# Kernel optimization log

Measured on AMD Instinct MI355X. Metric: run time of the kernel, lower is better.

## Reference

```python
import jax, jax.numpy as jnp
import numpy as np
import math

B, T, D = 2, 1024, 1024
H, K = 16, 64
THETA = 0.5
LAYER_ID, N_LAYERS = 4, 12
D_MIX, D_DECAY = 32, 64
LN_EPS = 1e-5 * 8.0 ** 2  # eps = 1e-5 * head_size_divisor**2


def setup_inputs() -> dict:
    key = jax.random.key(0)
    ks = jax.random.split(key, 10)
    x = jax.random.normal(ks[0], (B, T, D), jnp.float32)

    r01 = LAYER_ID / max(N_LAYERS - 1, 1)
    r1a0 = 1.0 - LAYER_ID / N_LAYERS
    ddd = (jnp.arange(D, dtype=jnp.float32) / D).reshape(1, 1, D)
    time_maa_x = 1.0 - ddd ** r1a0
    time_maa_w = 1.0 - ddd ** r1a0
    time_maa_k = 1.0 - ddd ** r1a0
    time_maa_v = 1.0 - (ddd ** r1a0 + 0.3 * r01)
    time_maa_r = 1.0 - ddd ** (0.5 * r1a0)
    time_maa_g = 1.0 - ddd ** (0.5 * r1a0)
    time_maa_w1 = jax.random.normal(ks[1], (D, D_MIX * 5), jnp.float32) * 0.01
    time_maa_w2 = jax.random.uniform(ks[2], (5, D_MIX, D), jnp.float32, -0.01, 0.01)

    n = jnp.arange(D, dtype=jnp.float32)
    time_decay = (-6.0 + 5.0 * (n / (D - 1)) ** (0.7 + 1.3 * r01)).reshape(1, 1, D)
    time_decay_w1 = jax.random.normal(ks[3], (D, D_DECAY), jnp.float32) * 0.01
    time_decay_w2 = jax.random.uniform(ks[4], (D_DECAY, D), jnp.float32, -0.01, 0.01)

    s = 1.0 / math.sqrt(D)
    W_r = jax.random.normal(ks[5], (D, D), jnp.float32) * s
    W_k = jax.random.normal(ks[6], (D, D), jnp.float32) * s
    W_v = jax.random.normal(ks[7], (D, D), jnp.float32) * s
    W_g = jax.random.normal(ks[8], (D, D), jnp.float32) * s
    W_o = jax.random.normal(ks[9], (D, D), jnp.float32) * s
    ln_gamma = jnp.ones((D,), jnp.float32)
    ln_beta = jnp.zeros((D,), jnp.float32)

    return dict(x=x, time_maa_x=time_maa_x, time_maa_w=time_maa_w,
                time_maa_k=time_maa_k, time_maa_v=time_maa_v,
                time_maa_r=time_maa_r, time_maa_g=time_maa_g,
                time_maa_w1=time_maa_w1, time_maa_w2=time_maa_w2,
                time_decay=time_decay, time_decay_w1=time_decay_w1,
                time_decay_w2=time_decay_w2, W_r=W_r, W_k=W_k, W_v=W_v,
                W_g=W_g, W_o=W_o, ln_gamma=ln_gamma, ln_beta=ln_beta)


def _bidir_token_shift(x):
    # bidirectional token shift: mean of previous and next token (zero-padded)
    prev = jnp.concatenate([jnp.zeros_like(x[:, :1]), x[:, :-1]], axis=1)
    nxt = jnp.concatenate([x[:, 1:], jnp.zeros_like(x[:, :1])], axis=1)
    return 0.5 * (prev + nxt)


def _lion_complex_attention(r, k, v, w, theta):
    # r,k,v,w: (B,H,T,K). Effective mask M[i,j] = exp-decay^|i-j| * cos(theta*|i-j|)
    cs = jnp.cumsum(w, axis=2)
    cs_b = cs - w
    cf = jnp.clip(cs - cs[:, :, T // 2:T // 2 + 1, :], -60.0, 60.0)
    cb = jnp.clip(cs_b - cs_b[:, :, T // 2:T // 2 + 1, :], -60.0, 60.0)
    t_idx = jnp.arange(T, dtype=jnp.float32)
    thF = (theta * (t_idx + 1.0)).reshape(1, 1, T, 1)
    thB = (theta * t_idx).reshape(1, 1, T, 1)
    exp_f, exp_nf = jnp.exp(cf), jnp.exp(-cf)
    exp_b, exp_nb = jnp.exp(cb), jnp.exp(-cb)
    mm = lambda a, b: jnp.einsum('bhik,bhjk->bhij', a, b)
    A_fwd = jnp.tril(mm(r * exp_f * jnp.cos(thF), k * exp_nf * jnp.cos(thF))
                     + mm(r * exp_f * jnp.sin(thF), k * exp_nf * jnp.sin(thF)))
    A_bwd = jnp.triu(mm(r * exp_nb * jnp.cos(thB), k * exp_b * jnp.cos(thB))
                     + mm(r * exp_nb * jnp.sin(thB), k * exp_b * jnp.sin(thB)), k=1)
    return (A_fwd + A_bwd) @ v  # (B,H,T,K)


def reference(x, time_maa_x, time_maa_w, time_maa_k, time_maa_v, time_maa_r,
              time_maa_g, time_maa_w1, time_maa_w2, time_decay, time_decay_w1,
              time_decay_w2, W_r, W_k, W_v, W_g, W_o, ln_gamma, ln_beta):
    dxprev = _bidir_token_shift(x) - x
    xxx = x + dxprev * time_maa_x
    t5 = jnp.tanh(xxx @ time_maa_w1).reshape(B, T, 5, D_MIX)
    m = jnp.einsum('btfm,fmd->fbtd', t5, time_maa_w2)  # (5,B,T,D)
    mw, mk, mv, mr, mg = m[0], m[1], m[2], m[3], m[4]
    xw = x + dxprev * (time_maa_w + mw)
    xk = x + dxprev * (time_maa_k + mk)
    xv = x + dxprev * (time_maa_v + mv)
    xr = x + dxprev * (time_maa_r + mr)
    xg = x + dxprev * (time_maa_g + mg)

    r = xr @ W_r
    k = xk @ W_k
    v = xv @ W_v
    g = jax.nn.silu(xg @ W_g)
    w = time_decay + jnp.tanh(xw @ time_decay_w1) @ time_decay_w2

    heads = lambda a: a.reshape(B, T, H, K).transpose(0, 2, 1, 3)
    r_h, k_h, v_h = heads(r), heads(k), heads(v)
    w_h = jnp.minimum(-jnp.exp(heads(w)), math.log(0.99))

    y = _lion_complex_attention(r_h, k_h, v_h, w_h, THETA)  # (B,H,T,K)
    y = y.transpose(0, 2, 1, 3).reshape(B * T, D)

    # GroupNorm(n_head groups) over channels
    yg = y.reshape(B * T, H, K)
    mu = yg.mean(axis=-1, keepdims=True)
    var = yg.var(axis=-1, keepdims=True)
    yn = ((yg - mu) / jnp.sqrt(var + LN_EPS)).reshape(B * T, D)
    y = (yn * ln_gamma + ln_beta).reshape(B, T, D)

    return (y * g) @ W_o
```

## Files before the change

### kernel.cpp

```cpp
#include <hip/hip_runtime.h>
#include <hip/hip_bf16.h>

using u16 = unsigned short;
using bf16x8 = __attribute__((ext_vector_type(8))) __bf16;
using f32x4  = __attribute__((ext_vector_type(4))) float;
using u16x4  = __attribute__((ext_vector_type(4))) u16;

#define DEV static __device__ __forceinline__

constexpr int Tn = 1024, Dn = 1024;

DEV u16 f2b(float f) { union { __hip_bfloat16 h; u16 u; } cv; cv.h = __float2bfloat16(f); return cv.u; }
DEV float b2f(u16 u) { union { unsigned i; float f; } cv; cv.i = (unsigned)u << 16; return cv.f; }
DEV void lds16(const void* g, void* s) {
    __builtin_amdgcn_global_load_lds(
        (const __attribute__((address_space(1))) void*)g,
        (__attribute__((address_space(3))) void*)s, 16, 0, 0);
}

__global__ __launch_bounds__(256) void k_shift(const float* __restrict__ x, const float* __restrict__ maa_x,
                                               float* __restrict__ dxp, u16* __restrict__ xxx) {
    long i4 = ((long)blockIdx.x * 256 + threadIdx.x) * 4;
    int t = (int)((i4 >> 10) & (Tn - 1));
    f32x4 xc = *(const f32x4*)(x + i4);
    f32x4 xp = {0.f, 0.f, 0.f, 0.f}, xn = {0.f, 0.f, 0.f, 0.f};
    if (t > 0)      xp = *(const f32x4*)(x + i4 - Dn);
    if (t < Tn - 1) xn = *(const f32x4*)(x + i4 + Dn);
    f32x4 dx = 0.5f * (xp + xn) - xc;
    *(f32x4*)(dxp + i4) = dx;
    f32x4 mx = *(const f32x4*)(maa_x + (i4 & (Dn - 1)));
    f32x4 v = xc + dx * mx;
    u16x4 o;
#pragma unroll
    for (int j = 0; j < 4; j++) o[j] = f2b(v[j]);
    *(u16x4*)(xxx + i4) = o;
}

__global__ __launch_bounds__(256) void k_transpose(const float* __restrict__ in,
                                                   u16* __restrict__ out, int R, int C) {
    __shared__ float tile[32][33];
    int c0 = blockIdx.x * 32, r0 = blockIdx.y * 32;
    int tx = threadIdx.x & 31, ty = threadIdx.x >> 5;
#pragma unroll
    for (int i = 0; i < 4; i++)
        tile[ty + i * 8][tx] = in[(long)(r0 + ty + i * 8) * C + c0 + tx];
    __syncthreads();
#pragma unroll
    for (int i = 0; i < 4; i++)
        out[(long)(c0 + ty + i * 8) * R + r0 + tx] = f2b(tile[tx][ty + i * 8]);
}

struct P5 { const float* p[5]; };
__global__ __launch_bounds__(256) void k_transpose5(P5 in, u16* __restrict__ out) {
    const float* src = in.p[blockIdx.z];
    u16* dst = out + (long)blockIdx.z * 1024 * 1024;
    __shared__ float tile[32][33];
    int c0 = blockIdx.x * 32, r0 = blockIdx.y * 32;
    int tx = threadIdx.x & 31, ty = threadIdx.x >> 5;
#pragma unroll
    for (int i = 0; i < 4; i++)
        tile[ty + i * 8][tx] = src[(long)(r0 + ty + i * 8) * 1024 + c0 + tx];
    __syncthreads();
#pragma unroll
    for (int i = 0; i < 4; i++)
        dst[(long)(c0 + ty + i * 8) * 1024 + r0 + tx] = f2b(tile[tx][ty + i * 8]);
}

enum { EPI_F32 = 0, EPI_TANH_F32, EPI_RKVG_BF16, EPI_TANH_BF16, EPI_DECAY_F32 };

template <int EPI, bool LOA = false>
__global__ __launch_bounds__(256) void k_gemm(const u16* __restrict__ A, const u16* __restrict__ A2,
                                              const u16* __restrict__ Bt,
                                              void* __restrict__ Cv, int M, int N, int K,
                                              long bA, long bB, long bC,
                                              const float* __restrict__ bias) {
    const u16* Ab = A + (long)blockIdx.z * bA;
    const u16* Bb = Bt + (long)blockIdx.z * bB;
    __shared__ __align__(16) u16 As[128 * 64];
    __shared__ __align__(16) u16 As2[LOA ? 128 * 64 : 8];
    __shared__ __align__(16) u16 Bs[128 * 64];
    int m0 = blockIdx.x * 128, n0 = blockIdx.y * 128;
    int tid = threadIdx.x, lane = tid & 63, wv = tid >> 6;
    int wm = (wv >> 1) * 64, wn = (wv & 1) * 64;
    f32x4 acc[4][4] = {};
    for (int k0 = 0; k0 < K; k0 += 64) {
        __syncthreads();
#pragma unroll
        for (int i = 0; i < 4; i++) {
            int c = tid + i * 256;
            int row = c >> 3;
            int grp = (c & 7) ^ (row & 7);
            long off = (long)row * K + k0 + grp * 8;
            lds16(Ab + (long)m0 * K + off, As + c * 8);
            if constexpr (LOA) lds16(A2 + (long)m0 * K + off, As2 + c * 8);
            lds16(Bb + (long)n0 * K + off, Bs + c * 8);
        }
        __syncthreads();
#pragma unroll
        for (int ksub = 0; ksub < 2; ksub++) {
            bf16x8 af[4], af2[4], bfv[4];
#pragma unroll
            for (int q = 0; q < 4; q++) {
                int row = wm + q * 16 + (lane & 15);
                int idx = (row * 64 + ksub * 32 + (lane >> 4) * 8) ^ ((row & 7) << 3);
                af[q] = *(const bf16x8*)(As + idx);
                if constexpr (LOA) af2[q] = *(const bf16x8*)(As2 + idx);
            }
#pragma unroll
            for (int q = 0; q < 4; q++) {
                int row = wn + q * 16 + (lane & 15);
                int idx = (row * 64 + ksub * 32 + (lane >> 4) * 8) ^ ((row & 7) << 3);
                bfv[q] = *(const bf16x8*)(Bs + idx);
            }
#pragma unroll
            for (int i = 0; i < 4; i++)
#pragma unroll
                for (int j = 0; j < 4; j++) {
                    acc[i][j] = __builtin_amdgcn_mfma_f32_16x16x32_bf16(af[i], bfv[j], acc[i][j], 0, 0, 0);
                    if constexpr (LOA)
                        acc[i][j] = __builtin_amdgcn_mfma_f32_16x16x32_bf16(af2[i], bfv[j], acc[i][j], 0, 0, 0);
                }
        }
    }
#pragma unroll
    for (int i = 0; i < 4; i++)
#pragma unroll
        for (int j = 0; j < 4; j++)
#pragma unroll
            for (int r = 0; r < 4; r++) {
                int gr = m0 + wm + i * 16 + ((lane >> 4) << 2) + r;
                int gc = n0 + wn + j * 16 + (lane & 15);
                if (gc < N) {
                    float v = acc[i][j][r];
                    long off = (long)blockIdx.z * bC + (long)gr * N + gc;
                    if constexpr (EPI == EPI_F32) ((float*)Cv)[off] = v;
                    else if constexpr (EPI == EPI_TANH_F32) ((float*)Cv)[off] = tanhf(v);
                    else if constexpr (EPI == EPI_RKVG_BF16) {
                        ((u16*)Cv)[off] = f2b((blockIdx.z == 3) ? v / (1.f + expf(-v)) : v);
                    }
                    else if constexpr (EPI == EPI_TANH_BF16) ((u16*)Cv)[off] = f2b(tanhf(v));
                    else if constexpr (EPI == EPI_DECAY_F32) {
                        float w = v + bias[gc];
                        ((float*)Cv)[off] = fminf(-expf(w), -0.010050335853501451f);
                    }
                }
            }
}

__global__ __launch_bounds__(256) void k_mixer(const float* __restrict__ x, const float* __restrict__ dxp,
                                               const float* __restrict__ t5, const float* __restrict__ w2,
                                               const float* __restrict__ maa_w, const float* __restrict__ maa_k,
                                               const float* __restrict__ maa_v, const float* __restrict__ maa_r,
                                               const float* __restrict__ maa_g, u16* __restrict__ xbuf) {
    __shared__ float t5s[32 * 160];
    __shared__ float w2s[160 * 64];
    int bt0 = blockIdx.x * 32, d0 = blockIdx.y * 64;
    int tid = threadIdx.x;
    for (int i = tid; i < 32 * 160; i += 256)
        t5s[i] = t5[(long)(bt0 + i / 160) * 160 + (i % 160)];
    for (int i = tid; i < 160 * 64; i += 256)
        w2s[i] = w2[(long)(i >> 6) * 1024 + d0 + (i & 63)];
    __syncthreads();
    int rr = tid >> 3, c8 = (tid & 7) * 8;
    int bt = bt0 + rr;
    float mv[5][8] = {};
#pragma unroll
    for (int f = 0; f < 5; f++)
        for (int mm = 0; mm < 32; mm++) {
            float tv = t5s[rr * 160 + f * 32 + mm];
#pragma unroll
            for (int dd = 0; dd < 8; dd++) mv[f][dd] += tv * w2s[(f * 32 + mm) * 64 + c8 + dd];
        }
    const float* maas[5] = {maa_r, maa_k, maa_v, maa_g, maa_w};
    const int fidx[5] = {3, 1, 2, 4, 0};
#pragma unroll
    for (int z = 0; z < 5; z++) {
#pragma unroll
        for (int dd = 0; dd < 8; dd++) {
            int d = d0 + c8 + dd;
            long ix = (long)bt * 1024 + d;
            float xc = x[ix], dx = dxp[ix];
            xbuf[(long)z * (2048L * 1024) + ix] = f2b(xc + dx * (maas[z][d] + mv[fidx[z]][dd]));
        }
    }
}

__global__ __launch_bounds__(256) void k_scan1(const float* __restrict__ wd, float* __restrict__ part) {
    int chunk = blockIdx.x;
    int idx = blockIdx.y * 256 + threadIdx.x;
    int b = idx >> 10, d = idx & 1023;
    const float* p = wd + ((long)(b * 1024 + chunk * 64)) * 1024 + d;
    float s = 0.f;
#pragma unroll
    for (int t = 0; t < 64; t++) s += p[(long)t * 1024];
    part[chunk * 2048 + idx] = s;
}

__global__ __launch_bounds__(256) void k_scan2(float* __restrict__ part) {
    int idx = blockIdx.x * 256 + threadIdx.x;
    float run = 0.f;
    for (int c = 0; c < 16; c++) {
        float p = part[c * 2048 + idx];
        part[c * 2048 + idx] = run;
        run += p;
    }
}

__global__ __launch_bounds__(256) void k_prep(const float* __restrict__ wd, const float* __restrict__ part,
                                              const u16* __restrict__ r, const u16* __restrict__ k,
                                              const u16* __restrict__ v, u16* __restrict__ Qf,
                                              u16* __restrict__ Kf, u16* __restrict__ Qb,
                                              u16* __restrict__ Kb, u16* __restrict__ Vt) {
    __shared__ float tcs[64][4];
    int chunk = blockIdx.x;
    if (threadIdx.x < 64) {
        int t = chunk * 64 + threadIdx.x;
        tcs[threadIdx.x][0] = cosf(0.5f * (float)(t + 1));
        tcs[threadIdx.x][1] = sinf(0.5f * (float)(t + 1));
        tcs[threadIdx.x][2] = cosf(0.5f * (float)t);
        tcs[threadIdx.x][3] = sinf(0.5f * (float)t);
    }
    __syncthreads();
    int idx = blockIdx.y * 256 + threadIdx.x;
    int b = idx >> 10, d = idx & 1023;
    int h = d >> 6, c = d & 63;
    float off8 = part[8 * 2048 + idx];
    float cs512 = off8 + wd[((long)b * 1024 + 512) * 1024 + d];
    float csb512 = off8;
    float run = part[chunk * 2048 + idx];
    long rowbase = ((long)b * 1024 + chunk * 64) * 1024 + d;
    int bh = b * 16 + h;
    long qbase = ((long)bh * 1024 + chunk * 64) * 128 + c;
    long vtbase = ((long)(bh * 64 + c)) * 1024 + chunk * 64;
    for (int tt = 0; tt < 64; tt++) {
        float wv_ = wd[rowbase + (long)tt * 1024];
        float csb = run;
        run += wv_;
        float cs = run;
        float ff = fminf(fmaxf(cs - cs512, -60.f), 60.f);
        float fb = fminf(fmaxf(csb - csb512, -60.f), 60.f);
        float ef = __expf(ff), enf = __expf(-ff), eb = __expf(fb), enb = __expf(-fb);
        float cF = tcs[tt][0], sF = tcs[tt][1], cB = tcs[tt][2], sB = tcs[tt][3];
        float rv = b2f(r[rowbase + (long)tt * 1024]);
        float kv = b2f(k[rowbase + (long)tt * 1024]);
        long q = qbase + (long)tt * 128;
        Qf[q] = f2b(rv * ef * cF);  Qf[q + 64] = f2b(rv * ef * sF);
        Kf[q] = f2b(kv * enf * cF); Kf[q + 64] = f2b(kv * enf * sF);
        Qb[q] = f2b(rv * enb * cB); Qb[q + 64] = f2b(rv * enb * sB);
        Kb[q] = f2b(kv * eb * cB);  Kb[q + 64] = f2b(kv * eb * sB);
        Vt[vtbase + tt] = v[rowbase + (long)tt * 1024];
    }
}

__global__ __launch_bounds__(256) void k_attn(const u16* __restrict__ Qf, const u16* __restrict__ Kf,
                                              const u16* __restrict__ Qb, const u16* __restrict__ Kb,
                                              const u16* __restrict__ Vt, float* __restrict__ Y) {
    __shared__ __align__(16) u16 lds[24576];
    u16* bufF = lds;
    u16* bufB = lds + 8192;
    u16* VS   = lds + 16384;
    u16* SS   = lds + 20480;
    int lin = blockIdx.y * 16 + blockIdx.x;
    int swz = (lin & 7) * 64 + (lin >> 3);
    int bh = swz >> 4, it = swz & 15;
    int i0 = it * 64;
    int tid = threadIdx.x, lane = tid & 63, wv = tid >> 6;
    const u16* QfG = Qf + (long)bh * Tn * 128;
    const u16* KfG = Kf + (long)bh * Tn * 128;
    const u16* QbG = Qb + (long)bh * Tn * 128;
    const u16* KbG = Kb + (long)bh * Tn * 128;
    const u16* VtG = Vt + (long)bh * 64 * Tn;

    {
        int4 qfr[4], qbr[4];
#pragma unroll
        for (int i = 0; i < 4; i++) {
            int c = tid + i * 256;
            qfr[i] = *(const int4*)(QfG + (long)(i0 + (c >> 4)) * 128 + (c & 15) * 8);
            qbr[i] = *(const int4*)(QbG + (long)(i0 + (c >> 4)) * 128 + (c & 15) * 8);
        }
#pragma unroll
        for (int i = 0; i < 4; i++) {
            int c = tid + i * 256;
            int d = (c * 8) ^ (((c >> 4) & 7) << 3);
            *(int4*)(bufF + d) = qfr[i];
            *(int4*)(bufB + d) = qbr[i];
        }
    }
    __syncthreads();
    bf16x8 qf[4], qb[4];
#pragma unroll
    for (int ks = 0; ks < 4; ks++) {
        int qidx = (((wv * 16 + (lane & 15)) * 128) + ks * 32 + (lane >> 4) * 8) ^ ((lane & 7) << 3);
        qf[ks] = *(const bf16x8*)(bufF + qidx);
        qb[ks] = *(const bf16x8*)(bufB + qidx);
    }
    f32x4 yacc[4] = {};
    for (int jt = 0; jt < 16; jt++) {
        int j0 = jt * 64;
        bool fwd = (jt <= it), bwd = (jt >= it);
        int4 kfr[4], kbr[4], vr[2];
        if (fwd) {
#pragma unroll
            for (int i = 0; i < 4; i++) {
                int c = tid + i * 256;
                kfr[i] = *(const int4*)(KfG + (long)(j0 + (c >> 4)) * 128 + (c & 15) * 8);
            }
        }
        if (bwd) {
#pragma unroll
            for (int i = 0; i < 4; i++) {
                int c = tid + i * 256;
                kbr[i] = *(const int4*)(KbG + (long)(j0 + (c >> 4)) * 128 + (c & 15) * 8);
            }
        }
#pragma unroll
        for (int i = 0; i < 2; i++) {
            int c = tid + i * 256;
            vr[i] = *(const int4*)(VtG + (long)(c >> 3) * Tn + j0 + (c & 7) * 8);
        }
        __syncthreads();
        if (fwd) {
#pragma unroll
            for (int i = 0; i < 4; i++) {
                int c = tid + i * 256;
                *(int4*)(bufF + ((c * 8) ^ (((c >> 4) & 7) << 3))) = kfr[i];
            }
        }
        if (bwd) {
#pragma unroll
            for (int i = 0; i < 4; i++) {
                int c = tid + i * 256;
                *(int4*)(bufB + ((c * 8) ^ (((c >> 4) & 7) << 3))) = kbr[i];
            }
        }
#pragma unroll
        for (int i = 0; i < 2; i++) {
            int c = tid + i * 256;
            *(int4*)(VS + ((c * 8) ^ (((c >> 3) & 7) << 3))) = vr[i];
        }
        __syncthreads();
        f32x4 sf[4] = {}, sb[4] = {};
        if (fwd) {
#pragma unroll
            for (int fn = 0; fn < 4; fn++)
#pragma unroll
                for (int ks = 0; ks < 4; ks++) {
                    int kidx = (((fn * 16 + (lane & 15)) * 128) + ks * 32 + (lane >> 4) * 8) ^ ((lane & 7) << 3);
                    bf16x8 kf = *(const bf16x8*)(bufF + kidx);
                    sf[fn] = __builtin_amdgcn_mfma_f32_16x16x32_bf16(qf[ks], kf, sf[fn], 0, 0, 0);
                }
        }
        if (bwd) {
#pragma unroll
            for (int fn = 0; fn < 4; fn++)
#pragma unroll
                for (int ks = 0; ks < 4; ks++) {
                    int kidx = (((fn * 16 + (lane & 15)) * 128) + ks * 32 + (lane >> 4) * 8) ^ ((lane & 7) << 3);
                    bf16x8 kb = *(const bf16x8*)(bufB + kidx);
                    sb[fn] = __builtin_amdgcn_mfma_f32_16x16x32_bf16(qb[ks], kb, sb[fn], 0, 0, 0);
                }
        }
#pragma unroll
        for (int fn = 0; fn < 4; fn++)
#pragma unroll
            for (int r = 0; r < 4; r++) {
                int li = wv * 16 + ((lane >> 4) << 2) + r;
                int lj = fn * 16 + (lane & 15);
                float s;
                if (jt < it) s = sf[fn][r];
                else if (jt > it) s = sb[fn][r];
                else s = (li >= lj) ? sf[fn][r] : sb[fn][r];
                SS[(li * 64 + lj) ^ ((li & 7) << 3)] = f2b(s);
            }
#pragma unroll
        for (int ks = 0; ks < 2; ks++) {
            int aidx = (((wv * 16 + (lane & 15)) * 64) + ks * 32 + (lane >> 4) * 8) ^ ((lane & 7) << 3);
            bf16x8 a = *(const bf16x8*)(SS + aidx);
#pragma unroll
            for (int fn = 0; fn < 4; fn++) {
                int bidx = (((fn * 16 + (lane & 15)) * 64) + ks * 32 + (lane >> 4) * 8) ^ ((lane & 7) << 3);
                bf16x8 bv = *(const bf16x8*)(VS + bidx);
                yacc[fn] = __builtin_amdgcn_mfma_f32_16x16x32_bf16(a, bv, yacc[fn], 0, 0, 0);
            }
        }
    }
    int b = bh >> 4, h = bh & 15;
    float* Yb = Y + (long)b * Tn * Dn + h * 64;
#pragma unroll
    for (int fn = 0; fn < 4; fn++)
#pragma unroll
        for (int r = 0; r < 4; r++)
            Yb[(long)(i0 + wv * 16 + ((lane >> 4) << 2) + r) * Dn + fn * 16 + (lane & 15)] = yacc[fn][r];
}

__global__ __launch_bounds__(256) void k_gnorm(const float* __restrict__ Y, const u16* __restrict__ G,
                                               const float* __restrict__ lng, const float* __restrict__ lnb,
                                               u16* __restrict__ YGhi, u16* __restrict__ YGlo) {
    int wv = threadIdx.x >> 6, lane = threadIdx.x & 63;
    int gidx = blockIdx.x * 4 + wv;
    int bt = gidx >> 4, h = gidx & 15;
    long base = (long)bt * 1024 + h * 64 + lane;
    float v = Y[base];
    float s = v;
#pragma unroll
    for (int m = 1; m < 64; m <<= 1) s += __shfl_xor(s, m, 64);
    float mean = s * (1.f / 64.f);
    float dv = v - mean;
    float q = dv * dv;
#pragma unroll
    for (int m = 1; m < 64; m <<= 1) q += __shfl_xor(q, m, 64);
    float var = q * (1.f / 64.f);
    float yn = dv * rsqrtf(var + 6.4e-4f);
    float o = yn * lng[h * 64 + lane] + lnb[h * 64 + lane];
    float og = o * b2f(G[base]);
    u16 hi = f2b(og);
    YGhi[base] = hi;
    YGlo[base] = f2b(og - b2f(hi));
}

extern "C" void kernel_launch(void* const* d_in, const int* in_sizes, int n_in,
                              void* d_out, int out_size, void* d_ws, size_t ws_size,
                              hipStream_t stream) {
    const float* x     = (const float*)d_in[0];
    const float* maa_x = (const float*)d_in[1];
    const float* maa_w = (const float*)d_in[2];
    const float* maa_k = (const float*)d_in[3];
    const float* maa_v = (const float*)d_in[4];
    const float* maa_r = (const float*)d_in[5];
    const float* maa_g = (const float*)d_in[6];
    const float* w1    = (const float*)d_in[7];
    const float* w2    = (const float*)d_in[8];
    const float* tdec  = (const float*)d_in[9];
    const float* dw1   = (const float*)d_in[10];
    const float* dw2   = (const float*)d_in[11];
    const float* Wr    = (const float*)d_in[12];
    const float* Wk    = (const float*)d_in[13];
    const float* Wv    = (const float*)d_in[14];
    const float* Wg    = (const float*)d_in[15];
    const float* Wo    = (const float*)d_in[16];
    const float* lng   = (const float*)d_in[17];
    const float* lnb   = (const float*)d_in[18];

    constexpr long MB = 1L << 20;
    if (ws_size < (size_t)(88 * MB)) {
        hipMemsetAsync(d_out, 0, (size_t)out_size * 4, stream);
        return;
    }
    char* ws = (char*)d_ws;
    u16*   WT    = (u16*)(ws + 0);
    u16*   w1T   = (u16*)(ws + 10 * MB);
    u16*   dw1T  = (u16*)(ws + 10 * MB + 512 * 1024);
    u16*   dw2T  = (u16*)(ws + 10 * MB + 768 * 1024);
    u16*   xxx   = (u16*)(ws + 11 * MB);
    float* t5    = (float*)(ws + 15 * MB);
    u16*   xbuf  = (u16*)(ws + 17 * MB);
    u16*   rbuf16 = (u16*)(ws + 37 * MB);
    u16*   kbuf16 = (u16*)(ws + 41 * MB);
    u16*   vbuf16 = (u16*)(ws + 45 * MB);
    u16*   gbuf16 = (u16*)(ws + 49 * MB);
    u16*   hbuf  = (u16*)(ws + 53 * MB);
    float* part  = (float*)(ws + 53 * MB + 256 * 1024);
    float* wdbuf = (float*)(ws + 54 * MB);
    u16*   QfB   = (u16*)(ws + 62 * MB);
    u16*   KfB   = (u16*)(ws + 70 * MB);
    float* dxp   = (float*)(ws + 78 * MB);
    u16*   QbB   = (u16*)(ws + 17 * MB);
    u16*   KbB   = (u16*)(ws + 25 * MB);
    u16*   VtB   = (u16*)(ws + 33 * MB);
    float* Ybuf  = (float*)(ws + 37 * MB);
    u16*   YGhi  = (u16*)(ws + 45 * MB);
    u16*   YGlo  = (u16*)(ws + 49 * MB);

    k_shift<<<2048, 256, 0, stream>>>(x, maa_x, dxp, xxx);
    P5 wp; wp.p[0] = Wr; wp.p[1] = Wk; wp.p[2] = Wv; wp.p[3] = Wg; wp.p[4] = Wo;
    k_transpose5<<<dim3(32, 32, 5), 256, 0, stream>>>(wp, WT);
    k_transpose<<<dim3(5, 32), 256, 0, stream>>>(w1, w1T, 1024, 160);
    k_transpose<<<dim3(2, 32), 256, 0, stream>>>(dw1, dw1T, 1024, 64);
    k_transpose<<<dim3(32, 2), 256, 0, stream>>>(dw2, dw2T, 64, 1024);

    k_gemm<EPI_TANH_F32><<<dim3(16, 2, 1), 256, 0, stream>>>(xxx, nullptr, w1T, t5, 2048, 160, 1024, 0, 0, 0, nullptr);
    k_mixer<<<dim3(64, 16), 256, 0, stream>>>(x, dxp, t5, w2, maa_w, maa_k, maa_v, maa_r, maa_g, xbuf);
    k_gemm<EPI_RKVG_BF16><<<dim3(16, 8, 4), 256, 0, stream>>>(xbuf, nullptr, WT, rbuf16, 2048, 1024, 1024,
                                                              2048L * 1024, 1024L * 1024, 2048L * 1024, nullptr);
    k_gemm<EPI_TANH_BF16><<<dim3(16, 1, 1), 256, 0, stream>>>(xbuf + 4L * 2048 * 1024, nullptr, dw1T, hbuf,
                                                              2048, 64, 1024, 0, 0, 0, nullptr);
    k_gemm<EPI_DECAY_F32><<<dim3(16, 8, 1), 256, 0, stream>>>(hbuf, nullptr, dw2T, wdbuf, 2048, 1024, 64, 0, 0, 0, tdec);

    k_scan1<<<dim3(16, 8), 256, 0, stream>>>(wdbuf, part);
    k_scan2<<<8, 256, 0, stream>>>(part);
    k_prep<<<dim3(16, 8), 256, 0, stream>>>(wdbuf, part, rbuf16, kbuf16, vbuf16, QfB, KfB, QbB, KbB, VtB);
    k_attn<<<dim3(16, 32), 256, 0, stream>>>(QfB, KfB, QbB, KbB, VtB, Ybuf);
    k_gnorm<<<8192, 256, 0, stream>>>(Ybuf, gbuf16, lng, lnb, YGhi, YGlo);
    k_gemm<EPI_F32, true><<<dim3(16, 8, 1), 256, 0, stream>>>(YGhi, YGlo, WT + 4L * 1024 * 1024, (float*)d_out,
                                                              2048, 1024, 1024, 0, 0, 0, nullptr);
    (void)in_sizes; (void)n_in; (void)out_size;
}
```

Baseline: 281.2 us.

## Split attention key range across two blocks and sum partials in groupnorm

The attention kernel gains a z-dimension of 2, with each block covering half of the key tiles, which doubles the grid from 512 to 1024 blocks to improve occupancy across CUs. Each half writes a separate fp32 partial output, and the groupnorm kernel adds the two partials before normalizing. Q loads are skipped when a block has no forward or backward tiles. The cost is an extra 8MB fp32 buffer write and read, plus duplicated Q loads across the split blocks.

```diff
diff --git a/kernel.cpp b/kernel.cpp
--- a/kernel.cpp
+++ b/kernel.cpp
@@ -254,7 +254,8 @@
 
 __global__ __launch_bounds__(256) void k_attn(const u16* __restrict__ Qf, const u16* __restrict__ Kf,
                                               const u16* __restrict__ Qb, const u16* __restrict__ Kb,
-                                              const u16* __restrict__ Vt, float* __restrict__ Y) {
+                                              const u16* __restrict__ Vt, float* __restrict__ Y0,
+                                              float* __restrict__ Y1) {
     __shared__ __align__(16) u16 lds[24576];
     u16* bufF = lds;
     u16* bufB = lds + 8192;
@@ -263,6 +264,9 @@
     int lin = blockIdx.y * 16 + blockIdx.x;
     int swz = (lin & 7) * 64 + (lin >> 3);
     int bh = swz >> 4, it = swz & 15;
+    int zz = blockIdx.z;
+    int jt0 = zz * 8, jt1 = jt0 + 8;
+    bool anyF = (it >= jt0), anyB = (it < jt1);
     int i0 = it * 64;
     int tid = threadIdx.x, lane = tid & 63, wv = tid >> 6;
     const u16* QfG = Qf + (long)bh * Tn * 128;
@@ -271,20 +275,30 @@
     const u16* KbG = Kb + (long)bh * Tn * 128;
     const u16* VtG = Vt + (long)bh * 64 * Tn;
 
-    {
-        int4 qfr[4], qbr[4];
+    if (anyF) {
+        int4 t[4];
 #pragma unroll
         for (int i = 0; i < 4; i++) {
             int c = tid + i * 256;
-            qfr[i] = *(const int4*)(QfG + (long)(i0 + (c >> 4)) * 128 + (c & 15) * 8);
-            qbr[i] = *(const int4*)(QbG + (long)(i0 + (c >> 4)) * 128 + (c & 15) * 8);
+            t[i] = *(const int4*)(QfG + (long)(i0 + (c >> 4)) * 128 + (c & 15) * 8);
         }
 #pragma unroll
         for (int i = 0; i < 4; i++) {
             int c = tid + i * 256;
-            int d = (c * 8) ^ (((c >> 4) & 7) << 3);
-            *(int4*)(bufF + d) = qfr[i];
-            *(int4*)(bufB + d) = qbr[i];
+            *(int4*)(bufF + ((c * 8) ^ (((c >> 4) & 7) << 3))) = t[i];
+        }
+    }
+    if (anyB) {
+        int4 t[4];
+#pragma unroll
+        for (int i = 0; i < 4; i++) {
+            int c = tid + i * 256;
+            t[i] = *(const int4*)(QbG + (long)(i0 + (c >> 4)) * 128 + (c & 15) * 8);
+        }
+#pragma unroll
+        for (int i = 0; i < 4; i++) {
+            int c = tid + i * 256;
+            *(int4*)(bufB + ((c * 8) ^ (((c >> 4) & 7) << 3))) = t[i];
         }
     }
     __syncthreads();
@@ -292,11 +306,11 @@
 #pragma unroll
     for (int ks = 0; ks < 4; ks++) {
         int qidx = (((wv * 16 + (lane & 15)) * 128) + ks * 32 + (lane >> 4) * 8) ^ ((lane & 7) << 3);
-        qf[ks] = *(const bf16x8*)(bufF + qidx);
-        qb[ks] = *(const bf16x8*)(bufB + qidx);
+        if (anyF) qf[ks] = *(const bf16x8*)(bufF + qidx);
+        if (anyB) qb[ks] = *(const bf16x8*)(bufB + qidx);
     }
     f32x4 yacc[4] = {};
-    for (int jt = 0; jt < 16; jt++) {
+    for (int jt = jt0; jt < jt1; jt++) {
         int j0 = jt * 64;
         bool fwd = (jt <= it), bwd = (jt >= it);
         int4 kfr[4], kbr[4], vr[2];
@@ -386,7 +400,7 @@
         }
     }
     int b = bh >> 4, h = bh & 15;
-    float* Yb = Y + (long)b * Tn * Dn + h * 64;
+    float* Yb = (zz ? Y1 : Y0) + (long)b * Tn * Dn + h * 64;
 #pragma unroll
     for (int fn = 0; fn < 4; fn++)
 #pragma unroll
@@ -394,14 +408,15 @@
             Yb[(long)(i0 + wv * 16 + ((lane >> 4) << 2) + r) * Dn + fn * 16 + (lane & 15)] = yacc[fn][r];
 }
 
-__global__ __launch_bounds__(256) void k_gnorm(const float* __restrict__ Y, const u16* __restrict__ G,
+__global__ __launch_bounds__(256) void k_gnorm(const float* __restrict__ Y0, const float* __restrict__ Y1,
+                                               const u16* __restrict__ G,
                                                const float* __restrict__ lng, const float* __restrict__ lnb,
                                                u16* __restrict__ YGhi, u16* __restrict__ YGlo) {
     int wv = threadIdx.x >> 6, lane = threadIdx.x & 63;
     int gidx = blockIdx.x * 4 + wv;
     int bt = gidx >> 4, h = gidx & 15;
     long base = (long)bt * 1024 + h * 64 + lane;
-    float v = Y[base];
+    float v = Y0[base] + Y1[base];
     float s = v;
 #pragma unroll
     for (int m = 1; m < 64; m <<= 1) s += __shfl_xor(s, m, 64);
@@ -469,6 +484,7 @@
     u16*   KbB   = (u16*)(ws + 25 * MB);
     u16*   VtB   = (u16*)(ws + 33 * MB);
     float* Ybuf  = (float*)(ws + 37 * MB);
+    float* Y1buf = (float*)(ws + 78 * MB);
     u16*   YGhi  = (u16*)(ws + 45 * MB);
     u16*   YGlo  = (u16*)(ws + 49 * MB);
 
@@ -490,8 +506,8 @@
     k_scan1<<<dim3(16, 8), 256, 0, stream>>>(wdbuf, part);
     k_scan2<<<8, 256, 0, stream>>>(part);
     k_prep<<<dim3(16, 8), 256, 0, stream>>>(wdbuf, part, rbuf16, kbuf16, vbuf16, QfB, KfB, QbB, KbB, VtB);
-    k_attn<<<dim3(16, 32), 256, 0, stream>>>(QfB, KfB, QbB, KbB, VtB, Ybuf);
-    k_gnorm<<<8192, 256, 0, stream>>>(Ybuf, gbuf16, lng, lnb, YGhi, YGlo);
+    k_attn<<<dim3(16, 32, 2), 256, 0, stream>>>(QfB, KfB, QbB, KbB, VtB, Ybuf, Y1buf);
+    k_gnorm<<<8192, 256, 0, stream>>>(Ybuf, Y1buf, gbuf16, lng, lnb, YGhi, YGlo);
     k_gemm<EPI_F32, true><<<dim3(16, 8, 1), 256, 0, stream>>>(YGhi, YGlo, WT + 4L * 1024 * 1024, (float*)d_out,
                                                               2048, 1024, 1024, 0, 0, 0, nullptr);
     (void)in_sizes; (void)n_in; (void)out_size;
```

Measured after the change: 289.1 us. 2.8% more time.
